# Kernel tuning notes

Hardware: AMD Instinct MI355X
Metric: run time of the kernel (lower is better)

## Reference

```python
import jax, jax.numpy as jnp
import numpy as np

DIM = 1024
HEADS = 16
SEQ_H = 32
SEQ_W = 32
HEAD_DIM = DIM // HEADS          # 64
ROT_DIM = HEAD_DIM // 4          # 16 per axis (lucidrains RotaryEmbedding dim)
FULL_ROT = 2 * ROT_DIM           # 32 channels rotated (axial: H-axis + W-axis)


def axial_freqs():
    # lucidrains 'pixel' mode: freqs = linspace(1, max_freq/2, dim//2) * pi, pos = linspace(-1, 1, steps)
    max_freq = SEQ_H * SEQ_W
    base = jnp.linspace(1.0, max_freq / 2.0, ROT_DIM // 2) * jnp.pi  # (rot//2,)
    th = jnp.linspace(-1.0, 1.0, SEQ_H)[:, None] * base[None, :]     # (H, rot//2)
    tw = jnp.linspace(-1.0, 1.0, SEQ_W)[:, None] * base[None, :]     # (W, rot//2)
    fh = jnp.repeat(th, 2, axis=-1)                                   # (H, rot)
    fw = jnpp_repeat = jnp.repeat(tw, 2, axis=-1)                     # (W, rot)
    fh = jnp.broadcast_to(fh[:, None, :], (SEQ_H, SEQ_W, ROT_DIM))
    fw = jnp.broadcast_to(fw[None, :, :], (SEQ_H, SEQ_W, ROT_DIM))
    return jnp.concatenate([fh, fw], axis=-1)                         # (H, W, FULL_ROT)


def rotate_half(t):
    # '... (d r) -> ... d r' with r=2, then (-x2, x1) interleaved back
    x = t.reshape(t.shape[:-1] + (t.shape[-1] // 2, 2))
    x1, x2 = x[..., 0], x[..., 1]
    return jnp.stack([-x2, x1], axis=-1).reshape(t.shape)


def apply_rope(t, cos, sin):
    # t: (B, heads, H, W, head_dim); only first FULL_ROT channels are rotated
    t_rot, t_pass = t[..., :FULL_ROT], t[..., FULL_ROT:]
    t_rot = t_rot * cos + rotate_half(t_rot) * sin
    return jnp.concatenate([t_rot, t_pass], axis=-1)


def setup_inputs() -> dict:
    key = jax.random.key(0)
    k1, k2, k3 = jax.random.split(key, 3)
    B, N = 8, SEQ_H * SEQ_W
    x = jax.random.normal(k1, (B, N, DIM), dtype=jnp.float32)
    Wqkv = jax.random.normal(k2, (3 * DIM, DIM), dtype=jnp.float32) * 0.02
    Wproj = jax.random.normal(k3, (DIM, DIM), dtype=jnp.float32) * 0.02
    bproj = jnp.zeros((DIM,), dtype=jnp.float32)
    return {"x": x, "Wqkv": Wqkv, "Wproj": Wproj, "bproj": bproj}


def reference(x, Wqkv, Wproj, bproj):
    B, N, C = x.shape
    qkv = jnp.einsum('bnc,fc->bnf', x, Wqkv)          # (B, N, 3C)
    q, k, v = jnp.split(qkv, 3, axis=-1)

    def to_grid(t):  # (B, N, C) -> (B, heads, H, W, hd)
        return t.reshape(B, SEQ_H, SEQ_W, HEADS, HEAD_DIM).transpose(0, 3, 1, 2, 4)

    q, k, v = to_grid(q), to_grid(k), to_grid(v)
    freqs = axial_freqs()
    cos, sin = jnp.cos(freqs), jnp.sin(freqs)         # (H, W, FULL_ROT)
    q = apply_rope(q, cos, sin)
    k = apply_rope(k, cos, sin)

    q = q.reshape(B, HEADS, N, HEAD_DIM)
    k = k.reshape(B, HEADS, N, HEAD_DIM)
    v = v.reshape(B, HEADS, N, HEAD_DIM)

    scale = 1.0 / jnp.sqrt(jnp.float32(HEAD_DIM))
    scores = jnp.einsum('bhqd,bhkd->bhqk', q, k) * scale
    attn = jax.nn.softmax(scores, axis=-1)
    out = jnp.einsum('bhqk,bhkd->bhqd', attn, v)       # (B, heads, N, hd)
    out = out.transpose(0, 2, 1, 3).reshape(B, N, C)
    return jnp.einsum('bnc,oc->bno', out, Wproj) + bproj
```

## Files before the change

### kernel.cpp

```cpp
#include <hip/hip_runtime.h>
#include <math.h>

#define DIM_ 1024
#define HEADS_ 16
#define HD_ 64
#define B_ 8
#define N_ 1024
#define M_TOT 8192

typedef __attribute__((ext_vector_type(4))) float f32x4;
typedef _Float16 v8h __attribute__((ext_vector_type(8)));
typedef __attribute__((ext_vector_type(4))) unsigned int u32x4;

static __device__ __forceinline__ unsigned short f2h(float x) {
  _Float16 h = (_Float16)x;
  return __builtin_bit_cast(unsigned short, h);
}
static __device__ __forceinline__ float fexp2(float x) {
  return __builtin_amdgcn_exp2f(x);
}
static __device__ __forceinline__ unsigned pkh2(float a, float b) {
  auto t = __builtin_amdgcn_cvt_pkrtz(a, b);
  return __builtin_bit_cast(unsigned, t);
}

static __device__ __forceinline__ void gload16(unsigned short* lds_base,
                                               const unsigned short* g) {
  __builtin_amdgcn_global_load_lds(
      (const __attribute__((address_space(1))) unsigned int*)g,
      (__attribute__((address_space(3))) unsigned int*)lds_base, 16, 0, 0);
}

__global__ __launch_bounds__(256) void split_all_k(
    const float* __restrict__ x, const float* __restrict__ wqkv,
    const float* __restrict__ wproj,
    unsigned short* __restrict__ xh, unsigned short* __restrict__ wqh,
    unsigned short* __restrict__ wph) {
  const int i = blockIdx.x * 256 + threadIdx.x;
  const float4* src;
  unsigned short* dst;
  int j;
  if (i < 2097152)      { j = i;           src = (const float4*)x;     dst = xh;  }
  else if (i < 2883584) { j = i - 2097152; src = (const float4*)wqkv;  dst = wqh; }
  else                  { j = i - 2883584; src = (const float4*)wproj; dst = wph; }
  float4 v = src[j];
  ushort4 h;
  h.x = f2h(v.x); h.y = f2h(v.y); h.z = f2h(v.z); h.w = f2h(v.w);
  ((ushort4*)dst)[j] = h;
}

__global__ void rope_table_k(float* cs, float* sn) {
  int i = threadIdx.x;
  if (i < 256) {
    int pos = i >> 3, j = i & 7;
    double u = -1.0 + (double)pos * (2.0/31.0);
    double ang = u * ((1.0 + 73.0*(double)j) * 3.14159265358979323846);
    cs[i] = (float)cos(ang);
    sn[i] = (float)sin(ang);
  }
}

static __device__ __forceinline__ void gemm_core2ph(
    const unsigned short* __restrict__ ah, const unsigned short* __restrict__ bh,
    unsigned short* SM,
    int m0, int f0, f32x4 acc[4][4]) {
  const int tid = threadIdx.x;
  const int w = tid >> 6, l = tid & 63;
  const int lg = l >> 4, lc = l & 15;
  const int wr = w >> 1, wc = w & 1;
  const int r64 = tid >> 2;
  const int ch  = tid & 3;
  const int wof = w * 512;
  const unsigned short* A = ah + (size_t)m0 * 1024;
  const unsigned short* B = bh + (size_t)f0 * 1024;

  auto stg = [&](const unsigned short* base, int t, unsigned short* dst) {
#pragma unroll
    for (int i = 0; i < 2; ++i) {
      const int row = i*64 + r64;
      const int sc = ch ^ ((row >> 1) & 3);
      gload16(dst + i*2048 + wof, base + (size_t)row*1024 + t*32 + sc*8);
    }
  };

  stg(A, 0, SM);
  stg(B, 0, SM + 4096);
  __syncthreads();
#pragma unroll 2
  for (int t = 0; t < 32; ++t) {
    unsigned short* cur = SM + (t & 1) * 8192;
    unsigned short* nxt = SM + ((t & 1) ^ 1) * 8192;
    if (t < 31) {
      stg(A, t + 1, nxt);
      stg(B, t + 1, nxt + 4096);
    }
    v8h a0[4], b0[4];
#pragma unroll
    for (int mi = 0; mi < 4; ++mi) {
      const int row = wr*64 + mi*16 + lc;
      a0[mi] = *(const v8h*)((const char*)cur + row*64 + ((lg ^ ((row >> 1) & 3)) << 4));
    }
#pragma unroll
    for (int nj = 0; nj < 4; ++nj) {
      const int row = wc*64 + nj*16 + lc;
      b0[nj] = *(const v8h*)((const char*)(cur + 4096) + row*64 + ((lg ^ ((row >> 1) & 3)) << 4));
    }
    __builtin_amdgcn_s_setprio(1);
#pragma unroll
    for (int mi = 0; mi < 4; ++mi)
#pragma unroll
      for (int nj = 0; nj < 4; ++nj)
        acc[mi][nj] = __builtin_amdgcn_mfma_f32_16x16x32_f16(a0[mi], b0[nj], acc[mi][nj], 0, 0, 0);
    __builtin_amdgcn_s_setprio(0);
    __syncthreads();
  }
}

__global__ __launch_bounds__(256) void qk_gemm_mfma(
    const unsigned short* __restrict__ xh,
    const unsigned short* __restrict__ wh,
    const float* __restrict__ cs, const float* __restrict__ sn,
    unsigned short* __restrict__ qh, unsigned short* __restrict__ kh) {
  __shared__ unsigned short SM[16384];
  const int tid = threadIdx.x;
  const int w = tid >> 6, l = tid & 63;
  const int lg = l >> 4, lc = l & 15;
  const int wr = w >> 1, wc = w & 1;
  const int nwg = gridDim.x * gridDim.y;
  int bid = blockIdx.y * gridDim.x + blockIdx.x;
  bid = (bid & 7) * (nwg >> 3) + (bid >> 3);
  const int m0 = (bid / gridDim.x) * 128;
  const int f0 = (bid % gridDim.x) * 128;
  f32x4 acc[4][4] = {};
  gemm_core2ph(xh, wh, SM, m0, f0, acc);
  const int qsel = f0 >> 10;
  const int head = ((f0 & 1023) >> 6) + wc;
  float* tbl = (float*)SM;
  tbl[tid] = cs[tid];
  tbl[256 + tid] = sn[tid];
  __syncthreads();
  const float scale = (qsel == 0) ? 0.18033688011112042f : 1.0f;
  unsigned short* oh = qsel ? kh : qh;
#pragma unroll
  for (int mi = 0; mi < 4; ++mi)
#pragma unroll
    for (int nj = 0; nj < 4; ++nj) {
      const int d = nj*16 + lc;
#pragma unroll
      for (int r = 0; r < 4; ++r) {
        const int m = m0 + wr*64 + mi*16 + lg*4 + r;
        const int b = m >> 10, n = m & 1023;
        float val = acc[mi][nj][r] * scale;
        float part = __shfl_xor(val, 1);
        if (nj < 2) {
          const int p = d >> 1;
          const int pos = (p < 8) ? (n >> 5) : (n & 31);
          const float c = tbl[pos*8 + (p & 7)];
          const float s = tbl[256 + pos*8 + (p & 7)];
          val = (d & 1) ? (val*c + part*s) : (val*c - part*s);
        }
        oh[((size_t)(b*HEADS_ + head)*N_ + n)*HD_ + d] = f2h(val);
      }
    }
}

__global__ __launch_bounds__(256) void v_gemm_mfma(
    const unsigned short* __restrict__ xh, const unsigned short* __restrict__ wh,
    unsigned short* __restrict__ vth) {
  __shared__ unsigned short SM[18432];
  const int tid = threadIdx.x;
  const int w = tid >> 6, l = tid & 63;
  const int lg = l >> 4, lc = l & 15;
  const int wr = w >> 1, wc = w & 1;
  const int nwg = gridDim.x * gridDim.y;
  int bid = blockIdx.y * gridDim.x + blockIdx.x;
  bid = (bid & 7) * (nwg >> 3) + (bid >> 3);
  const int m0 = (bid / gridDim.x) * 128;
  const int f0 = (bid % gridDim.x) * 128;
  f32x4 acc[4][4] = {};
  gemm_core2ph(xh, wh + (size_t)2048*1024, SM, m0, f0, acc);
  __syncthreads();
  unsigned short* VT = SM + w * 4608;
#pragma unroll
  for (int mi = 0; mi < 4; ++mi)
#pragma unroll
    for (int nj = 0; nj < 4; ++nj)
#pragma unroll
      for (int r = 0; r < 4; r += 2) {
        const int ml = mi*16 + lg*4 + r;
        const int dl = nj*16 + lc;
        *(unsigned*)((char*)VT + dl*144 + ml*2) = pkh2(acc[mi][nj][r], acc[mi][nj][r+1]);
      }
  __syncthreads();
  const int b = m0 >> 10;
  const int n0 = (m0 & 1023) + wr*64;
  const int head = (f0 >> 6) + wc;
#pragma unroll
  for (int j = 0; j < 8; ++j) {
    const int dl = (l >> 3) + j*8;
    u32x4 val = *(const u32x4*)((const char*)VT + dl*144 + (l & 7)*16);
    *(u32x4*)(vth + ((size_t)((b*HEADS_ + head)*HD_ + dl))*N_ + n0 + (l & 7)*8) = val;
  }
}

__global__ __launch_bounds__(256) void proj_gemm_mfma(
    const unsigned short* __restrict__ ah,
    const unsigned short* __restrict__ wh,
    const float* __restrict__ bias, float* __restrict__ out) {
  __shared__ unsigned short SM[16384];
  const int tid = threadIdx.x;
  const int w = tid >> 6, l = tid & 63;
  const int lg = l >> 4, lc = l & 15;
  const int wr = w >> 1, wc = w & 1;
  const int nwg = gridDim.x * gridDim.y;
  int bid = blockIdx.y * gridDim.x + blockIdx.x;
  bid = (bid & 7) * (nwg >> 3) + (bid >> 3);
  const int m0 = (bid / gridDim.x) * 128;
  const int o0 = (bid % gridDim.x) * 128;
  f32x4 acc[4][4] = {};
  gemm_core2ph(ah, wh, SM, m0, o0, acc);
#pragma unroll
  for (int nj = 0; nj < 4; ++nj) {
    const int o = o0 + wc*64 + nj*16 + lc;
    const float bv = bias[o];
#pragma unroll
    for (int mi = 0; mi < 4; ++mi)
#pragma unroll
      for (int r = 0; r < 4; ++r) {
        const int m = m0 + wr*64 + mi*16 + lg*4 + r;
        out[(size_t)m*DIM_ + o] = acc[mi][nj][r] + bv;
      }
  }
}

__global__ __launch_bounds__(256, 5) void attn_mfma_k(
    const unsigned short* __restrict__ qh,
    const unsigned short* __restrict__ kh,
    const unsigned short* __restrict__ vth,
    unsigned short* __restrict__ aoh) {
  __shared__ unsigned short KhS[8192];
  __shared__ unsigned short VhS[8192];
  const int tid = threadIdx.x;
  const int w = tid >> 6, l = tid & 63;
  const int lg = l >> 4, lc = l & 15;
  const int bh = blockIdx.x, qt = blockIdx.y;
  const size_t gb = (size_t)bh * (N_*HD_);

  v8h qf[2];
#pragma unroll
  for (int c = 0; c < 2; ++c)
    qf[c] = *(const v8h*)(qh + gb +
        (size_t)(qt*64 + w*16 + lc)*HD_ + c*32 + lg*8);
  f32x4 O[4];
#pragma unroll
  for (int dt = 0; dt < 4; ++dt) O[dt] = (f32x4){0.f, 0.f, 0.f, 0.f};
  float lrow = 0.f;

  const int wof = w * 512;
  const int kpr = tid >> 3;
  const int ksc = (tid & 7) ^ (kpr & 7);
  const int vr  = tid >> 4;
  const int vsc = (tid & 15) ^ (vr & 15);

  for (int t = 0; t < 8; ++t) {
#pragma unroll
    for (int i = 0; i < 4; ++i) {
      const int p = i*32 + kpr;
      const int kap = ((p >> 5) << 5) | (((p >> 2) & 3) << 3)
                    | (((p >> 4) & 1) << 2) | (p & 3);
      gload16(KhS + i*2048 + wof, kh + gb + (size_t)(t*128 + kap)*HD_ + ksc*8);
      const int row = i*16 + vr;
      gload16(VhS + i*2048 + wof, vth + gb + (size_t)row*N_ + t*128 + vsc*8);
    }
    __syncthreads();
#pragma unroll
    for (int h = 0; h < 2; ++h) {
      f32x4 s[4];
      __builtin_amdgcn_s_setprio(1);
#pragma unroll
      for (int k4 = 0; k4 < 4; ++k4) {
        s[k4] = (f32x4){0.f, 0.f, 0.f, 0.f};
        const int row = (h*4 + k4)*16 + lc;
        const int sw = (row & 7) << 4;
#pragma unroll
        for (int c = 0; c < 2; ++c) {
          v8h kf = *(const v8h*)((const char*)KhS + row*128 + ((c*64 + lg*16) ^ sw));
          s[k4] = __builtin_amdgcn_mfma_f32_16x16x32_f16(kf, qf[c], s[k4], 0, 0, 0);
        }
      }
      __builtin_amdgcn_s_setprio(0);
      u32x4 pa[2];
#pragma unroll
      for (int cc = 0; cc < 2; ++cc) {
        const float p0 = fexp2(s[2*cc][0]);
        const float p1 = fexp2(s[2*cc][1]);
        const float p2 = fexp2(s[2*cc][2]);
        const float p3 = fexp2(s[2*cc][3]);
        const float p4 = fexp2(s[2*cc+1][0]);
        const float p5 = fexp2(s[2*cc+1][1]);
        const float p6 = fexp2(s[2*cc+1][2]);
        const float p7 = fexp2(s[2*cc+1][3]);
        lrow += ((p0 + p1) + (p2 + p3)) + ((p4 + p5) + (p6 + p7));
        pa[cc] = (u32x4){pkh2(p0, p1), pkh2(p2, p3), pkh2(p4, p5), pkh2(p6, p7)};
      }
      __builtin_amdgcn_s_setprio(1);
#pragma unroll
      for (int dt = 0; dt < 4; ++dt) {
        const int row = dt*16 + lc;
        const int sw = (row & 15) << 4;
#pragma unroll
        for (int cc = 0; cc < 2; ++cc) {
          const int c = h*2 + cc;
          v8h vf = *(const v8h*)((const char*)VhS + row*256 + ((c*64 + lg*16) ^ sw));
          O[dt] = __builtin_amdgcn_mfma_f32_16x16x32_f16(
              __builtin_bit_cast(v8h, pa[cc]), vf, O[dt], 0, 0, 0);
        }
      }
      __builtin_amdgcn_s_setprio(0);
    }
    __syncthreads();
  }
  lrow += __shfl_xor(lrow, 16);
  lrow += __shfl_xor(lrow, 32);
  const int b = bh >> 4, h = bh & 15;
  const float myinv = 1.0f / lrow;
#pragma unroll
  for (int r = 0; r < 4; ++r) {
    const float iv = __shfl(myinv, lg*4 + r);
    const int n = qt*64 + w*16 + lg*4 + r;
    const size_t base = ((size_t)(b*N_ + n))*DIM_ + h*HD_ + lc;
#pragma unroll
    for (int dt = 0; dt < 4; ++dt)
      aoh[base + dt*16] = f2h(O[dt][r] * iv);
  }
}

extern "C" void kernel_launch(void* const* d_in, const int* in_sizes, int n_in,
                              void* d_out, int out_size, void* d_ws, size_t ws_size,
                              hipStream_t stream) {
  const float* x     = (const float*)d_in[0];
  const float* Wqkv  = (const float*)d_in[1];
  const float* Wproj = (const float*)d_in[2];
  const float* bproj = (const float*)d_in[3];
  float* out = (float*)d_out;

  unsigned short* xh  = (unsigned short*)d_ws;
  unsigned short* wqh = xh  + 8388608;
  unsigned short* wph = wqh + 3145728;
  unsigned short* qh  = wph + 1048576;
  unsigned short* kh  = qh  + 8388608;
  unsigned short* vth = kh  + 8388608;
  float* cs = (float*)(vth + 8388608);
  float* sn = cs + 256;
  unsigned short* aoh = xh;

  hipLaunchKernelGGL(rope_table_k, dim3(1), dim3(256), 0, stream, cs, sn);
  hipLaunchKernelGGL(split_all_k, dim3(12288), dim3(256), 0, stream,
                     x, Wqkv, Wproj, xh, wqh, wph);
  hipLaunchKernelGGL(qk_gemm_mfma, dim3(16, 64), dim3(256), 0, stream,
                     xh, wqh, cs, sn, qh, kh);
  hipLaunchKernelGGL(v_gemm_mfma, dim3(8, 64), dim3(256), 0, stream, xh, wqh, vth);
  hipLaunchKernelGGL(attn_mfma_k, dim3(128, 16), dim3(256), 0, stream,
                     qh, kh, vth, aoh);
  hipLaunchKernelGGL(proj_gemm_mfma, dim3(8, 64), dim3(256), 0, stream,
                     aoh, wph, bproj, out);
}
```

Baseline: 161.6 us.

## Fuse Q/K and V projection GEMMs into one launch with staged coalesced stores

Merges the separate QK and V projection kernels into a single 24x64-block kernel, where blocks covering the V columns branch to a transposed store path. The Q/K epilogue now stages the RoPE-rotated fp16 tile through XOR-swizzled shared memory and writes 16-byte vectors per row instead of scattered 2-byte stores. The rope cos/sin values are read from global memory rather than a shared-memory copy, and the V transpose buffer uses a swizzle in place of padding. This removes one kernel launch and its tail, and fills the GPU with one larger grid; in exchange the kernel has a divergent epilogue and more global loads for the rope table.

Result: slower. 168.0 us (+4.0%).

```diff
diff --git a/kernel.cpp b/kernel.cpp
--- a/kernel.cpp
+++ b/kernel.cpp
@@ -116,11 +116,12 @@
   }
 }
 
-__global__ __launch_bounds__(256) void qk_gemm_mfma(
+__global__ __launch_bounds__(256) void qkv_gemm_mfma(
     const unsigned short* __restrict__ xh,
     const unsigned short* __restrict__ wh,
     const float* __restrict__ cs, const float* __restrict__ sn,
-    unsigned short* __restrict__ qh, unsigned short* __restrict__ kh) {
+    unsigned short* __restrict__ qh, unsigned short* __restrict__ kh,
+    unsigned short* __restrict__ vth) {
   __shared__ unsigned short SM[16384];
   const int tid = threadIdx.x;
   const int w = tid >> 6, l = tid & 63;
@@ -134,13 +135,34 @@
   f32x4 acc[4][4] = {};
   gemm_core2ph(xh, wh, SM, m0, f0, acc);
   const int qsel = f0 >> 10;
-  const int head = ((f0 & 1023) >> 6) + wc;
-  float* tbl = (float*)SM;
-  tbl[tid] = cs[tid];
-  tbl[256 + tid] = sn[tid];
-  __syncthreads();
+  const int b = m0 >> 10;
+
+  if (qsel == 2) {
+    unsigned short* VT = SM + w * 4096;
+#pragma unroll
+    for (int mi = 0; mi < 4; ++mi)
+#pragma unroll
+      for (int nj = 0; nj < 4; ++nj)
+#pragma unroll
+        for (int r = 0; r < 4; r += 2) {
+          const int ml = mi*16 + lg*4 + r;
+          const int dl = nj*16 + lc;
+          const int addr = dl*128 + (((ml >> 3) ^ (dl & 7)) << 4) + (ml & 7)*2;
+          *(unsigned*)((char*)VT + addr) = pkh2(acc[mi][nj][r], acc[mi][nj][r+1]);
+        }
+    const int n0 = (m0 & 1023) + wr*64;
+    const int head = ((f0 - 2048) >> 6) + wc;
+#pragma unroll
+    for (int j = 0; j < 8; ++j) {
+      const int dl = (l >> 3) + j*8;
+      const int c = (l & 7) ^ (dl & 7);
+      u32x4 val = *(const u32x4*)((const char*)VT + dl*128 + c*16);
+      *(u32x4*)(vth + ((size_t)((b*HEADS_ + head)*HD_ + dl))*N_ + n0 + (l & 7)*8) = val;
+    }
+    return;
+  }
+
   const float scale = (qsel == 0) ? 0.18033688011112042f : 1.0f;
-  unsigned short* oh = qsel ? kh : qh;
 #pragma unroll
   for (int mi = 0; mi < 4; ++mi)
 #pragma unroll
@@ -148,58 +170,42 @@
       const int d = nj*16 + lc;
 #pragma unroll
       for (int r = 0; r < 4; ++r) {
-        const int m = m0 + wr*64 + mi*16 + lg*4 + r;
-        const int b = m >> 10, n = m & 1023;
         float val = acc[mi][nj][r] * scale;
-        float part = __shfl_xor(val, 1);
+        const float part = __shfl_xor(val, 1);
         if (nj < 2) {
+          const int m = m0 + wr*64 + mi*16 + lg*4 + r;
+          const int n = m & 1023;
           const int p = d >> 1;
           const int pos = (p < 8) ? (n >> 5) : (n & 31);
-          const float c = tbl[pos*8 + (p & 7)];
-          const float s = tbl[256 + pos*8 + (p & 7)];
+          const float c = cs[pos*8 + (p & 7)];
+          const float s = sn[pos*8 + (p & 7)];
           val = (d & 1) ? (val*c + part*s) : (val*c - part*s);
         }
-        oh[((size_t)(b*HEADS_ + head)*N_ + n)*HD_ + d] = f2h(val);
-      }
-    }
-}
-
-__global__ __launch_bounds__(256) void v_gemm_mfma(
-    const unsigned short* __restrict__ xh, const unsigned short* __restrict__ wh,
-    unsigned short* __restrict__ vth) {
-  __shared__ unsigned short SM[18432];
-  const int tid = threadIdx.x;
-  const int w = tid >> 6, l = tid & 63;
-  const int lg = l >> 4, lc = l & 15;
-  const int wr = w >> 1, wc = w & 1;
-  const int nwg = gridDim.x * gridDim.y;
-  int bid = blockIdx.y * gridDim.x + blockIdx.x;
-  bid = (bid & 7) * (nwg >> 3) + (bid >> 3);
-  const int m0 = (bid / gridDim.x) * 128;
-  const int f0 = (bid % gridDim.x) * 128;
-  f32x4 acc[4][4] = {};
-  gemm_core2ph(xh, wh + (size_t)2048*1024, SM, m0, f0, acc);
+        acc[mi][nj][r] = val;
+      }
+    }
+#pragma unroll
+  for (int mi = 0; mi < 4; ++mi)
+#pragma unroll
+    for (int nj = 0; nj < 4; ++nj)
+#pragma unroll
+      for (int r = 0; r < 4; ++r) {
+        const int g = wr*64 + mi*16 + lg*4 + r;
+        const int col = wc*64 + nj*16 + lc;
+        const int addr = g*256 + (((col >> 3) ^ (g & 15)) << 4) + (col & 7)*2;
+        *(unsigned short*)((char*)SM + addr) = f2h(acc[mi][nj][r]);
+      }
   __syncthreads();
-  unsigned short* VT = SM + w * 4608;
-#pragma unroll
-  for (int mi = 0; mi < 4; ++mi)
-#pragma unroll
-    for (int nj = 0; nj < 4; ++nj)
-#pragma unroll
-      for (int r = 0; r < 4; r += 2) {
-        const int ml = mi*16 + lg*4 + r;
-        const int dl = nj*16 + lc;
-        *(unsigned*)((char*)VT + dl*144 + ml*2) = pkh2(acc[mi][nj][r], acc[mi][nj][r+1]);
-      }
-  __syncthreads();
-  const int b = m0 >> 10;
-  const int n0 = (m0 & 1023) + wr*64;
-  const int head = (f0 >> 6) + wc;
+  unsigned short* oh = qsel ? kh : qh;
+  const int g = tid >> 1, hh = tid & 1;
+  const int head = ((f0 & 1023) >> 6) + hh;
+  const int n = (m0 & 1023) + g;
+  const size_t base = ((size_t)(b*HEADS_ + head)*N_ + n)*HD_;
 #pragma unroll
   for (int j = 0; j < 8; ++j) {
-    const int dl = (l >> 3) + j*8;
-    u32x4 val = *(const u32x4*)((const char*)VT + dl*144 + (l & 7)*16);
-    *(u32x4*)(vth + ((size_t)((b*HEADS_ + head)*HD_ + dl))*N_ + n0 + (l & 7)*8) = val;
+    const int cl = hh*8 + j;
+    u32x4 val = *(const u32x4*)((const char*)SM + g*256 + ((cl ^ (g & 15)) << 4));
+    *(u32x4*)(oh + base + j*8) = val;
   }
 }
 
@@ -357,9 +363,8 @@
   hipLaunchKernelGGL(rope_table_k, dim3(1), dim3(256), 0, stream, cs, sn);
   hipLaunchKernelGGL(split_all_k, dim3(12288), dim3(256), 0, stream,
                      x, Wqkv, Wproj, xh, wqh, wph);
-  hipLaunchKernelGGL(qk_gemm_mfma, dim3(16, 64), dim3(256), 0, stream,
-                     xh, wqh, cs, sn, qh, kh);
-  hipLaunchKernelGGL(v_gemm_mfma, dim3(8, 64), dim3(256), 0, stream, xh, wqh, vth);
+  hipLaunchKernelGGL(qkv_gemm_mfma, dim3(24, 64), dim3(256), 0, stream,
+                     xh, wqh, cs, sn, qh, kh, vth);
   hipLaunchKernelGGL(attn_mfma_k, dim3(128, 16), dim3(256), 0, stream,
                      qh, kh, vth, aoh);
   hipLaunchKernelGGL(proj_gemm_mfma, dim3(8, 64), dim3(256), 0, stream,
```
